# Kernel tuning notes

Hardware: AMD Instinct MI355X
Metric: run time of the kernel (lower is better)

Reference implementation:

```python
import jax, jax.numpy as jnp
import numpy as np

B, NV, NDIRS, NRINGS, NCH, NF = 2, 15000, 16, 3, 32, 64


def setup_inputs() -> dict:
    key = jax.random.key(0)
    k1, k2, k3, k4 = jax.random.split(key, 4)
    y = jax.random.normal(k1, (B, NV, NDIRS, NCH), dtype=jnp.float32)
    ft_v = jax.random.randint(k2, (NV, NRINGS, NDIRS), 0, NV, dtype=jnp.int32)
    ft_d = jax.random.randint(k3, (NV, NRINGS, NDIRS), 0, NDIRS, dtype=jnp.int32)
    kernel = jax.random.normal(k4, (NRINGS, NDIRS, NCH, NF), dtype=jnp.float32) * 0.05
    bias = jnp.zeros((NF,), dtype=jnp.float32)
    return {"y": y, "ft_v": ft_v, "ft_d": ft_d, "kernel": kernel, "bias": bias}


def reference(y, ft_v, ft_d, kernel, bias):
    # y: [b, nv, ndirs, nch]; ft_v/ft_d: [nv, nrings, ndirs]; kernel: [nrings, ndirs, nch, nf]
    b, nv, ndirs, nch = y.shape
    f = jnp.transpose(y, (1, 2, 3, 0))  # [nv, ndirs, nch, b]
    dirs = jnp.arange(ndirs)

    def per_dir(l):
        # cyclic forward shift of the direction axis, composed with the
        # frame-transporter gather: z[v,r,d,c,b] = f[ft_v[v,r,d], (ft_d[v,r,d]+l)%n, c, b]
        d_idx = (ft_d + l) % ndirs                # [nv, nrings, ndirs]
        z = f[ft_v, d_idx]                        # [nv, nrings, ndirs, nch, b]
        # kernel shifted in reverse: k_l[:, d] = kernel[:, (d-l)%n]
        k_l = kernel[:, (dirs - l) % ndirs]       # [nrings, ndirs, nch, nf]
        return jnp.einsum('vrdcb,rdcf->vbf', z, k_l)  # [nv, b, nf]

    out = jax.lax.map(per_dir, dirs)              # [ndirs, nv, b, nf] (sequential, like tf.while_loop)
    out = jnp.transpose(out, (2, 1, 0, 3))        # [b, nv, ndirs, nf]
    out = out + bias
    return jax.nn.relu(out)
```

## Files before the change

### kernel.cpp

```cpp
#include <hip/hip_runtime.h>

#define NV 15000
#define ND 16
#define NR 3
#define NC 32
#define NFDIM 64
#define BB 2

typedef short bf16x8 __attribute__((ext_vector_type(8)));
typedef float f32x4 __attribute__((ext_vector_type(4)));
typedef unsigned short u16x8 __attribute__((ext_vector_type(8)));

#define KB_OFF     30720000u
#define WS_NEEDED  30916608u

__device__ __forceinline__ unsigned short f2bf(float x) {
  union { float f; unsigned int u; } cv; cv.f = x;
  unsigned int u = cv.u;
  u += 0x7FFF + ((u >> 16) & 1);
  return (unsigned short)(u >> 16);
}

__global__ void prep_y(const float* __restrict__ y, u16x8* __restrict__ yt) {
  int tid = blockIdx.x * 256 + threadIdx.x;
  if (tid >= (NV * ND * BB * NC) / 8) return;
  int o   = tid * 8;
  int v   = o >> 10;
  int rem = o & 1023;
  int d   = rem >> 6;
  int b   = (rem >> 5) & 1;
  int c0  = rem & 31;
  const f32x4* src = (const f32x4*)(y + (((b * NV + v) * ND + d) * NC + c0));
  f32x4 lo = src[0], hi = src[1];
  u16x8 r;
#pragma unroll
  for (int i = 0; i < 4; i++) { r[i] = f2bf(lo[i]); r[4 + i] = f2bf(hi[i]); }
  yt[tid] = r;
}

__global__ void prep_kb(const float* __restrict__ kern, unsigned short* __restrict__ kb) {
  int t = blockIdx.x * 256 + threadIdx.x;
  if (t >= 48 * 4 * 64) return;
  int lane  = t & 63;
  int ft    = (t >> 6) & 3;
  int chunk = t >> 8;
  int q = lane >> 4;
  int f = (lane & 15) * 4 + ft;
  unsigned short* dst = kb + t * 8;
#pragma unroll
  for (int j = 0; j < 8; j++) {
    int k = q * 8 + j;
    dst[j] = f2bf(kern[(chunk * NC + k) * NFDIM + f]);
  }
}

__global__ __launch_bounds__(256, 3) void sync_conv_main(
    const unsigned short* __restrict__ yt, const unsigned short* __restrict__ kb,
    const int* __restrict__ ftv, const int* __restrict__ ftd,
    const float* __restrict__ bias, float* __restrict__ out) {
  __shared__ int pidx[16][49];
  __shared__ int pre[4][16][49];

  int tid  = threadIdx.x;
  int lane = tid & 63;
  int w    = tid >> 6;
  int mg   = blockIdx.x >> 2;
  int lg   = blockIdx.x & 3;
  int l    = lg * 4 + w;
  int vbase = mg * 16;

  for (int t = tid; t < 16 * 48; t += 256) {
    int i = t / 48, j = t - i * 48;
    int v = vbase + i; v = v < NV ? v : NV - 1;
    pidx[i][j] = ftv[v * 48 + j] * 16 + (ftd[v * 48 + j] & 15);
  }
  __syncthreads();
#pragma unroll
  for (int wl = 0; wl < 4; wl++) {
    int ll = lg * 4 + wl;
    for (int t = tid; t < 768; t += 256) {
      int i = t / 48, j = t - i * 48;
      int p = pidx[i][j];
      pre[wl][i][j] = (p >> 4) * 1024 + ((((p & 15) + ll) & 15) << 6);
    }
  }
  __syncthreads();

  int q    = lane >> 4;
  int n    = lane & 15;
  int voff = n >> 1;
  int lane_elem = (n & 1) * 32 + q * 8;
  const unsigned short* kb_lane = kb + lane * 8;
  const int* pre_w0 = &pre[w][voff][0];
  const int* pre_w1 = &pre[w][8 + voff][0];

  f32x4 acc[2][4];
#pragma unroll
  for (int i = 0; i < 2; i++)
#pragma unroll
    for (int j = 0; j < 4; j++) acc[i][j] = (f32x4){0.f, 0.f, 0.f, 0.f};

  bf16x8 bufA[3][2][2];
  bf16x8 bufB[2][2][4];

  auto loadB = [&](int bt, int par) {
#pragma unroll
    for (int ds = 0; ds < 2; ds++) {
      int s = 2 * bt + ds;
      const unsigned short* kbp = kb_lane + s * 2048;
#pragma unroll
      for (int ft = 0; ft < 4; ft++)
        bufB[par][ds][ft] = *reinterpret_cast<const bf16x8*>(kbp + ft * 512);
    }
  };
  auto loadA = [&](int bt, int par) {
#pragma unroll
    for (int ds = 0; ds < 2; ds++) {
      int s = 2 * bt + ds;
      int j = (s & 48) | ((s + l) & 15);
      int o0 = pre_w0[j] + lane_elem;
      int o1 = pre_w1[j] + lane_elem;
      bufA[par][0][ds] = *reinterpret_cast<const bf16x8*>(yt + o0);
      bufA[par][1][ds] = *reinterpret_cast<const bf16x8*>(yt + o1);
    }
  };
  auto compute = [&](int parA, int parB) {
    __builtin_amdgcn_s_setprio(1);
#pragma unroll
    for (int ds = 0; ds < 2; ds++)
#pragma unroll
      for (int mt = 0; mt < 2; mt++)
#pragma unroll
        for (int ft = 0; ft < 4; ft++)
          acc[mt][ft] = __builtin_amdgcn_mfma_f32_16x16x32_bf16(
              bufA[parA][mt][ds], bufB[parB][ds][ft], acc[mt][ft], 0, 0, 0);
    __builtin_amdgcn_s_setprio(0);
  };

  loadA(0, 0);
  loadB(0, 0);
  loadA(1, 1);
  __builtin_amdgcn_sched_barrier(0);

#pragma unroll
  for (int bt = 0; bt < 24; bt++) {
    if (bt + 1 < 24) loadB(bt + 1, (bt + 1) & 1);
    if (bt + 2 < 24) loadA(bt + 2, (bt + 2) % 3);
    __builtin_amdgcn_sched_barrier(0);
    compute(bt % 3, bt & 1);
    __builtin_amdgcn_sched_barrier(0);
  }

  f32x4 bv = *reinterpret_cast<const f32x4*>(bias + 4 * n);

#pragma unroll
  for (int mt = 0; mt < 2; mt++) {
#pragma unroll
    for (int reg = 0; reg < 4; reg++) {
      int m  = q * 4 + reg;
      int v  = vbase + mt * 8 + (m >> 1);
      int bb = m & 1;
      if (v < NV) {
        f32x4 x;
#pragma unroll
        for (int ft = 0; ft < 4; ft++) {
          float t = acc[mt][ft][reg] + bv[ft];
          x[ft] = t > 0.f ? t : 0.f;
        }
        float* dst = out + (((bb * NV + v) * ND + l) * NFDIM) + 4 * n;
        __builtin_nontemporal_store(x, (f32x4*)dst);
      }
    }
  }
}

__global__ void fallback_kernel(const float* __restrict__ y, const int* __restrict__ ftv,
                                const int* __restrict__ ftd, const float* __restrict__ kern,
                                const float* __restrict__ bias, float* __restrict__ out) {
  int idx = blockIdx.x;
  int l = idx & 15;
  int v = (idx >> 4) % NV;
  int b = idx / (NV * ND);
  int f = threadIdx.x;
  float acc = 0.f;
  for (int r = 0; r < NR; r++)
    for (int d = 0; d < ND; d++) {
      int ii = (v * NR + r) * ND + d;
      int vv = ftv[ii];
      int dd = (ftd[ii] + l) & 15;
      int dp = (d - l) & 15;
      const float* yp = y + ((b * NV + vv) * ND + dd) * NC;
      const float* kp = kern + ((r * 16 + dp) * NC) * NFDIM + f;
#pragma unroll 8
      for (int c = 0; c < NC; c++) acc += yp[c] * kp[c * NFDIM];
    }
  float x = acc + bias[f];
  out[idx * NFDIM + f] = x > 0.f ? x : 0.f;
}

extern "C" void kernel_launch(void* const* d_in, const int* in_sizes, int n_in,
                              void* d_out, int out_size, void* d_ws, size_t ws_size,
                              hipStream_t stream) {
  const float* y    = (const float*)d_in[0];
  const int*   ftv  = (const int*)d_in[1];
  const int*   ftd  = (const int*)d_in[2];
  const float* kern = (const float*)d_in[3];
  const float* bias = (const float*)d_in[4];
  float* out = (float*)d_out;

  if (ws_size >= (size_t)WS_NEEDED) {
    char* ws = (char*)d_ws;
    unsigned short* yt = (unsigned short*)ws;
    unsigned short* kb = (unsigned short*)(ws + KB_OFF);

    prep_y<<<(NV * ND * BB * NC / 8 + 255) / 256, 256, 0, stream>>>(y, (u16x8*)yt);
    prep_kb<<<(48 * 4 * 64 + 255) / 256, 256, 0, stream>>>(kern, kb);
    sync_conv_main<<<3752, 256, 0, stream>>>(yt, kb, ftv, ftd, bias, out);
  } else {
    fallback_kernel<<<BB * NV * ND, NFDIM, 0, stream>>>(y, ftv, ftd, kern, bias, out);
  }
}
```

Baseline: 371.2 us.

## Stage shared kernel weights through LDS via async global_load_lds triple buffering

The four waves in a block previously each loaded the same kernel-weight fragments from global memory into registers. Now each wave copies a quarter of each weight tile into a three-slot LDS ring using global_load_lds, with vmcnt waits and a block barrier per step, and reads the B fragments from LDS. The gathered A operands are now loaded synchronously inside the step instead of two steps ahead, and launch bounds are raised to four blocks per SM to cut register pressure. The trade is less redundant global traffic for a barrier every step and A-load latency that is no longer hidden by a software pipeline.

```diff
diff --git a/kernel.cpp b/kernel.cpp
--- a/kernel.cpp
+++ b/kernel.cpp
@@ -10,9 +10,14 @@
 typedef short bf16x8 __attribute__((ext_vector_type(8)));
 typedef float f32x4 __attribute__((ext_vector_type(4)));
 typedef unsigned short u16x8 __attribute__((ext_vector_type(8)));
+typedef unsigned int u32;
 
 #define KB_OFF     30720000u
 #define WS_NEEDED  30916608u
+
+#define AS1 __attribute__((address_space(1)))
+#define AS3 __attribute__((address_space(3)))
+#define GLOAD16(gp, lp) __builtin_amdgcn_global_load_lds((AS1 const u32*)(gp), (AS3 u32*)(lp), 16, 0, 0)
 
 __device__ __forceinline__ unsigned short f2bf(float x) {
   union { float f; unsigned int u; } cv; cv.f = x;
@@ -54,12 +59,13 @@
   }
 }
 
-__global__ __launch_bounds__(256, 3) void sync_conv_main(
+__global__ __launch_bounds__(256, 4) void sync_conv_main(
     const unsigned short* __restrict__ yt, const unsigned short* __restrict__ kb,
     const int* __restrict__ ftv, const int* __restrict__ ftd,
     const float* __restrict__ bias, float* __restrict__ out) {
-  __shared__ int pidx[16][49];
-  __shared__ int pre[4][16][49];
+  __shared__ int   pidx[16][49];
+  __shared__ int   pre[4][16][49];
+  __shared__ short lds_b[3 * 4096];
 
   int tid  = threadIdx.x;
   int lane = tid & 63;
@@ -90,7 +96,6 @@
   int n    = lane & 15;
   int voff = n >> 1;
   int lane_elem = (n & 1) * 32 + q * 8;
-  const unsigned short* kb_lane = kb + lane * 8;
   const int* pre_w0 = &pre[w][voff][0];
   const int* pre_w1 = &pre[w][8 + voff][0];
 
@@ -100,55 +105,50 @@
 #pragma unroll
     for (int j = 0; j < 4; j++) acc[i][j] = (f32x4){0.f, 0.f, 0.f, 0.f};
 
-  bf16x8 bufA[3][2][2];
-  bf16x8 bufB[2][2][4];
-
-  auto loadB = [&](int bt, int par) {
+  auto stageB = [&](int t, int slot) {
+    const unsigned short* g = kb + t * 4096 + w * 1024 + (lane << 3);
+    short* d = lds_b + slot * 4096 + w * 1024;
+    GLOAD16(g, d);
+    GLOAD16(g + 512, d + 512);
+  };
+
+  stageB(0, 0);
+  stageB(1, 1);
+
+  int sl = 0;
+#pragma unroll 3
+  for (int t = 0; t < 24; t++) {
+    if (t < 23) {
+      asm volatile("s_waitcnt vmcnt(2)" ::: "memory");
+    } else {
+      asm volatile("s_waitcnt vmcnt(0)" ::: "memory");
+    }
+    __builtin_amdgcn_s_barrier();
+
+    bf16x8 A[2][2];
 #pragma unroll
     for (int ds = 0; ds < 2; ds++) {
-      int s = 2 * bt + ds;
-      const unsigned short* kbp = kb_lane + s * 2048;
-#pragma unroll
-      for (int ft = 0; ft < 4; ft++)
-        bufB[par][ds][ft] = *reinterpret_cast<const bf16x8*>(kbp + ft * 512);
-    }
-  };
-  auto loadA = [&](int bt, int par) {
+      int s = 2 * t + ds;
+      int j = (s & 48) | ((s + l) & 15);
+      A[0][ds] = *reinterpret_cast<const bf16x8*>(yt + pre_w0[j] + lane_elem);
+      A[1][ds] = *reinterpret_cast<const bf16x8*>(yt + pre_w1[j] + lane_elem);
+    }
+
+    if (t + 2 < 24) stageB(t + 2, sl == 0 ? 2 : sl - 1);
+
+    const short* lb = lds_b + sl * 4096;
+    __builtin_amdgcn_s_setprio(1);
 #pragma unroll
     for (int ds = 0; ds < 2; ds++) {
-      int s = 2 * bt + ds;
-      int j = (s & 48) | ((s + l) & 15);
-      int o0 = pre_w0[j] + lane_elem;
-      int o1 = pre_w1[j] + lane_elem;
-      bufA[par][0][ds] = *reinterpret_cast<const bf16x8*>(yt + o0);
-      bufA[par][1][ds] = *reinterpret_cast<const bf16x8*>(yt + o1);
-    }
-  };
-  auto compute = [&](int parA, int parB) {
-    __builtin_amdgcn_s_setprio(1);
-#pragma unroll
-    for (int ds = 0; ds < 2; ds++)
-#pragma unroll
-      for (int mt = 0; mt < 2; mt++)
-#pragma unroll
-        for (int ft = 0; ft < 4; ft++)
-          acc[mt][ft] = __builtin_amdgcn_mfma_f32_16x16x32_bf16(
-              bufA[parA][mt][ds], bufB[parB][ds][ft], acc[mt][ft], 0, 0, 0);
+#pragma unroll
+      for (int ft = 0; ft < 4; ft++) {
+        bf16x8 bf = *reinterpret_cast<const bf16x8*>(lb + ds * 2048 + ft * 512 + (lane << 3));
+        acc[0][ft] = __builtin_amdgcn_mfma_f32_16x16x32_bf16(A[0][ds], bf, acc[0][ft], 0, 0, 0);
+        acc[1][ft] = __builtin_amdgcn_mfma_f32_16x16x32_bf16(A[1][ds], bf, acc[1][ft], 0, 0, 0);
+      }
+    }
     __builtin_amdgcn_s_setprio(0);
-  };
-
-  loadA(0, 0);
-  loadB(0, 0);
-  loadA(1, 1);
-  __builtin_amdgcn_sched_barrier(0);
-
-#pragma unroll
-  for (int bt = 0; bt < 24; bt++) {
-    if (bt + 1 < 24) loadB(bt + 1, (bt + 1) & 1);
-    if (bt + 2 < 24) loadA(bt + 2, (bt + 2) % 3);
-    __builtin_amdgcn_sched_barrier(0);
-    compute(bt % 3, bt & 1);
-    __builtin_amdgcn_sched_barrier(0);
+    sl = sl == 2 ? 0 : sl + 1;
   }
 
   f32x4 bv = *reinterpret_cast<const f32x4*>(bias + 4 * n);
```

Measured after the change: 364.7 us. Within noise of the previous version (-1.8%).
